# Performance work log

Measured on AMD Instinct MI355X. Metric: run time of the kernel, lower is better.

Reference implementation:

```python
import jax, jax.numpy as jnp
import numpy as np

B, N, C, H, D, K = 4, 8192, 384, 12, 2, 32
M = N // K            # 256 members per cluster
CH = C // H // 2      # 16 = q/k head dim (v gets 2*head_dim per the 6-way split)


def setup_inputs() -> dict:
    key = jax.random.key(0)
    ks = jax.random.split(key, 8)
    pos = jax.random.uniform(ks[0], (B, N, D), jnp.float32)
    feat = jax.random.normal(ks[1], (B, N, C), jnp.float32)
    # per-(b*h) row permutation of 0..N-1 -> clusters partition all tokens (cluster_mask=None path)
    perm_keys = jax.random.split(ks[2], B * H)
    member_idx = jax.vmap(lambda kk: jax.random.permutation(kk, N))(perm_keys).reshape(B * H, K, M)
    w_qkv = jax.random.normal(ks[3], (3 * C, C), jnp.float32) * (C ** -0.5)
    b_qkv = jnp.zeros((3 * C,), jnp.float32)
    w_pos = jax.random.normal(ks[4], (H, D), jnp.float32) * 0.1   # Conv1d(h*d->h, ksize 1, groups=h) weight squeezed
    b_pos = jnp.zeros((H,), jnp.float32)
    w_proj = jax.random.normal(ks[5], (C, 2 * C), jnp.float32) * ((2 * C) ** -0.5)
    b_proj = jnp.zeros((C,), jnp.float32)
    return {"pos": pos, "feat": feat, "member_idx": member_idx,
            "w_qkv": w_qkv, "b_qkv": b_qkv, "w_pos": w_pos, "b_pos": b_pos,
            "w_proj": w_proj, "b_proj": b_proj}


def reference(pos, feat, member_idx, w_qkv, b_qkv, w_pos, b_pos, w_proj, b_proj):
    b, n, c = feat.shape
    d = pos.shape[2]
    bh, k, m = member_idx.shape
    h = bh // b
    ch = c // h // 2
    scale = (c // h) ** -0.5

    # qkv projection -> (b*h, n, 6, ch)
    qkv = feat @ w_qkv.T + b_qkv                      # b n 3c
    qkv = qkv.reshape(b, n, h, 6, ch).transpose(0, 2, 1, 3, 4).reshape(bh, n, 6, ch)

    # gather cluster members -> (b*k, h, m, 6, ch)
    row = jnp.arange(bh)[:, None, None]
    g = qkv[row, member_idx]                          # bh k m 6 ch
    g = g.reshape(b, h, k, m, 6, ch).transpose(0, 2, 1, 3, 4, 5).reshape(b * k, h, m, 6, ch)
    q = g[:, :, :, 0] * scale                         # bk h m ch
    kk = g[:, :, :, 1]                                # bk h m ch
    v = g[:, :, :, 2:].reshape(b * k, h, m, 4 * ch)   # bk h m 2c_

    attn = jnp.einsum('khic,khjc->khij', q, kk)       # bk h m m (k axis = b*k)

    # positional bias: kernel-1 grouped conv is linear -> bias[i,j] = s_j - s_i + b_pos
    pos_n = pos / pos.reshape(-1, d).max(0)           # b n d
    pos_bh = jnp.repeat(pos_n, h, axis=0)             # bh n d
    pos_g = pos_bh[row, member_idx]                   # bh k m d
    pos_g = pos_g.reshape(b, h, k, m, d).transpose(0, 2, 1, 3, 4).reshape(b * k, h, m, d)
    s = jnp.einsum('khmd,hd->khm', pos_g, w_pos)      # bk h m
    pos_bias = s[:, :, None, :] - s[:, :, :, None] + b_pos[None, :, None, None]

    attn = jax.nn.softmax(attn + pos_bias, axis=-1)
    out = jnp.einsum('khij,khjc->khic', attn, v)      # bk h m 2c_

    # scatter back to original token order (member_idx is a permutation per row)
    out = out.reshape(b, k, h, m, 4 * ch).transpose(0, 2, 1, 3, 4).reshape(bh, k * m, 4 * ch)
    new_feat = jnp.zeros((bh, n, 4 * ch), out.dtype)
    new_feat = new_feat.at[jnp.arange(bh)[:, None], member_idx.reshape(bh, k * m)].set(out)
    feat2 = new_feat.reshape(b, h, n, 4 * ch).transpose(0, 2, 1, 3).reshape(b, n, 2 * c)

    return feat2 @ w_proj.T + b_proj                  # b n c
```

## Files before the change

kernel.cpp:

```cpp
#include <hip/hip_runtime.h>
#include <hip/hip_bf16.h>

#define B_  4
#define N_  8192
#define C_  384
#define H_  12
#define K_  32
#define M_  256
#define BN_ (B_*N_)
#define QKVD 1152
#define VSTR 260
#define LOG2E 1.4426950408889634f


typedef __attribute__((ext_vector_type(8)))  short  bf16x8;
typedef __attribute__((ext_vector_type(4)))  float  f32x4;
typedef __attribute__((ext_vector_type(16))) float  f32x16;
typedef __attribute__((ext_vector_type(4)))  ushort ushort4v;
typedef __attribute__((ext_vector_type(8)))  ushort ushort8v;

#define GLOBAL_AS __attribute__((address_space(1)))
#define LDS_AS    __attribute__((address_space(3)))

__device__ __forceinline__ void load_lds_16B(const ushort* g, ushort* l) {
    __builtin_amdgcn_global_load_lds((const GLOBAL_AS unsigned int*)g,
                                     (LDS_AS unsigned int*)l, 16, 0, 0);
}
__device__ __forceinline__ unsigned cvtpk_bf16(float lo, float hi) {
    unsigned r;
    asm("v_cvt_pk_bf16_f32 %0, %1, %2" : "=v"(r) : "v"(lo), "v"(hi));
    return r;
}
__device__ __forceinline__ float exp2_fast(float x) {
    float r;
    asm("v_exp_f32 %0, %1" : "=v"(r) : "v"(x));
    return r;
}
__device__ __forceinline__ float rcp_fast(float x) {
    float r;
    asm("v_rcp_f32 %0, %1" : "=v"(r) : "v"(x));
    return r;
}

__global__ void posmax_kernel(const float* __restrict__ pos, unsigned* __restrict__ pmax) {
    int tid = blockIdx.x * blockDim.x + threadIdx.x;
    float m0 = 0.f, m1 = 0.f;
    for (int i = tid; i < BN_; i += gridDim.x * blockDim.x) {
        m0 = fmaxf(m0, pos[(size_t)i * 2 + 0]);
        m1 = fmaxf(m1, pos[(size_t)i * 2 + 1]);
    }
    #pragma unroll
    for (int off = 32; off; off >>= 1) {
        m0 = fmaxf(m0, __shfl_down(m0, off));
        m1 = fmaxf(m1, __shfl_down(m1, off));
    }
    __shared__ float s0[4], s1[4];
    int w = threadIdx.x >> 6;
    if ((threadIdx.x & 63) == 0) { s0[w] = m0; s1[w] = m1; }
    __syncthreads();
    if (threadIdx.x == 0) {
        for (int i = 1; i < 4; i++) { m0 = fmaxf(m0, s0[i]); m1 = fmaxf(m1, s1[i]); }
        atomicMax(&pmax[0], __float_as_uint(m0));
        atomicMax(&pmax[1], __float_as_uint(m1));
    }
}

__global__ __launch_bounds__(256) void cast_kernel(const float* __restrict__ src,
                                                   ushort* __restrict__ dst, int n4) {
    int i = blockIdx.x * blockDim.x + threadIdx.x;
    if (i >= n4) return;
    float4 a = reinterpret_cast<const float4*>(src)[i];
    unsigned u01 = cvtpk_bf16(a.x, a.y), u23 = cvtpk_bf16(a.z, a.w);
    ushort4 o = { (ushort)(u01 & 0xffff), (ushort)(u01 >> 16),
                  (ushort)(u23 & 0xffff), (ushort)(u23 >> 16) };
    reinterpret_cast<ushort4*>(dst)[i] = o;
}

#define WQN 110592
#define WPN 73728
__global__ __launch_bounds__(256) void cast_w(const float* __restrict__ wq,
                                              const float* __restrict__ wp,
                                              ushort* __restrict__ wqb,
                                              ushort* __restrict__ wpb) {
    int i = blockIdx.x * 256 + threadIdx.x;
    const float* src; ushort* dst; int j;
    if (i < WQN) { src = wq; dst = wqb; j = i; }
    else         { src = wp; dst = wpb; j = i - WQN; }
    float4 a = reinterpret_cast<const float4*>(src)[j];
    unsigned u01 = cvtpk_bf16(a.x, a.y), u23 = cvtpk_bf16(a.z, a.w);
    ushort4 o = { (ushort)(u01 & 0xffff), (ushort)(u01 >> 16),
                  (ushort)(u23 & 0xffff), (ushort)(u23 >> 16) };
    reinterpret_cast<ushort4*>(dst)[j] = o;
}

__global__ __launch_bounds__(256) void gemm_qkv_s(const ushort* __restrict__ A,
                                                  const ushort* __restrict__ Bw,
                                                  const float* __restrict__ bias,
                                                  ushort* __restrict__ qkv) {
    constexpr int NB = QKVD / 128;
    __shared__ ushort As[128 * 64];
    __shared__ ushort Bs[128 * 64];
    const int wgid = blockIdx.x;
    const int xcd  = wgid & 7;
    const int loc  = wgid >> 3;
    const int bm = (xcd * 32 + loc / NB) * 128;
    const int bn = (loc % NB) * 128;
    const int t = threadIdx.x;
    const int l = t & 63;
    const int wr = (t >> 6) >> 1, wc = (t >> 6) & 1;
    const int fr = l & 15, fq = l >> 4;

    f32x4 zero = {0.f, 0.f, 0.f, 0.f};
    f32x4 acc[4][4];
    #pragma unroll
    for (int m = 0; m < 4; m++)
        #pragma unroll
        for (int n = 0; n < 4; n++) acc[m][n] = zero;

    for (int k0 = 0; k0 < 384; k0 += 64) {
        #pragma unroll
        for (int i = 0; i < 4; i++) {
            int elem = (i * 256 + t) * 8;
            int row = elem >> 6, kk = elem & 63;
            int kks = kk ^ ((row & 7) << 3);
            load_lds_16B(A + (size_t)(bm + row) * 384 + k0 + kks, &As[elem]);
        }
        #pragma unroll
        for (int i = 0; i < 4; i++) {
            int elem = (i * 256 + t) * 8;
            int row = elem >> 6, kk = elem & 63;
            int kks = kk ^ ((row & 7) << 3);
            load_lds_16B(Bw + (size_t)(bn + row) * 384 + k0 + kks, &Bs[elem]);
        }
        __syncthreads();
        #pragma unroll
        for (int kk = 0; kk < 64; kk += 32) {
            bf16x8 af[4], bfr[4];
            #pragma unroll
            for (int m = 0; m < 4; m++) {
                int row = wr * 64 + m * 16 + fr;
                af[m] = *reinterpret_cast<const bf16x8*>(&As[row * 64 + ((kk + fq * 8) ^ ((row & 7) << 3))]);
            }
            #pragma unroll
            for (int n = 0; n < 4; n++) {
                int row = wc * 64 + n * 16 + fr;
                bfr[n] = *reinterpret_cast<const bf16x8*>(&Bs[row * 64 + ((kk + fq * 8) ^ ((row & 7) << 3))]);
            }
            #pragma unroll
            for (int m = 0; m < 4; m++)
                #pragma unroll
                for (int n = 0; n < 4; n++)
                    acc[m][n] = __builtin_amdgcn_mfma_f32_16x16x32_bf16(af[m], bfr[n], acc[m][n], 0, 0, 0);
        }
        __syncthreads();
    }
    const int bq = bm >> 13;
    const int nbase = bm & (N_ - 1);
    #pragma unroll
    for (int n = 0; n < 4; n++) {
        int col = bn + wc * 64 + n * 16 + fr;
        int hc = col / 96, cn = col % 96;
        float bc = bias[col];
        ushort* base = qkv + ((size_t)(bq * H_ + hc) * N_ + nbase) * 96 + cn;
        #pragma unroll
        for (int m = 0; m < 4; m++) {
            #pragma unroll
            for (int r = 0; r < 4; r++) {
                int rowoff = wr * 64 + m * 16 + fq * 4 + r;
                __hip_bfloat16 hv = __float2bfloat16(acc[m][n][r] + bc);
                base[(size_t)rowoff * 96] = *(const ushort*)&hv;
            }
        }
    }
}

__global__ __launch_bounds__(512, 1) void attn_kernel(const ushort* __restrict__ qkv,
                                                      const int* __restrict__ member_idx,
                                                      const float* __restrict__ pos,
                                                      const float* __restrict__ w_pos,
                                                      const unsigned* __restrict__ pmax_u,
                                                      ushort* __restrict__ feat2) {
    const int id = blockIdx.x;
    const int bh = (id >> 8) * 8 + (id & 7);
    const int kc = (id >> 3) & 31;
    const int b = bh / H_, h = bh % H_;
    __shared__ ushort Ks[M_ * 16];
    __shared__ ushort Vt[64 * VSTR];
    __shared__ float  SpA[M_];
    __shared__ int    Idx[M_];
    __shared__ float  dinvS[8 * 32];

    const int t  = threadIdx.x;
    const int w  = t >> 6, l = t & 63;
    const int hi = l >> 5, ln = l & 31;
    const int* mi = member_idx + (((size_t)b * H_ + h) * K_ + kc) * M_;
    const ushort* slab = qkv + (size_t)bh * N_ * 96;
    const size_t rowbase = (size_t)b * N_;
    const float scale2 = 0.17677669529663687f * LOG2E;

    const int iq = 32 * w + ln;
    const int nq = mi[iq];
    bf16x8 qf = *(const bf16x8*)(slab + (size_t)nq * 96 + hi * 8);
    const int u = t >> 2, cq = t & 3;
    const int n0 = mi[2 * u], n1 = mi[2 * u + 1];
    const ushort* s0 = slab + (size_t)n0 * 96 + 32 + cq * 16;
    const ushort* s1 = slab + (size_t)n1 * 96 + 32 + cq * 16;
    ushort8v v0a = *(const ushort8v*)s0;
    ushort8v v0b = *(const ushort8v*)(s0 + 8);
    ushort8v v1a = *(const ushort8v*)s1;
    ushort8v v1b = *(const ushort8v*)(s1 + 8);
    {
        int row = t >> 1, half = t & 1;
        int n = mi[row];
        load_lds_16B(slab + (size_t)n * 96 + 16 + half * 8, &Ks[t * 8]);
    }
    if (t < M_) {
        int n = mi[t];
        Idx[t] = n;
        float inv0 = rcp_fast(__uint_as_float(pmax_u[0]));
        float inv1 = rcp_fast(__uint_as_float(pmax_u[1]));
        float sp = pos[(rowbase + n) * 2 + 0] * inv0 * w_pos[h * 2 + 0]
                 + pos[(rowbase + n) * 2 + 1] * inv1 * w_pos[h * 2 + 1];
        int jj = t & 31, jt = t >> 5;
        int r  = (jj & 3) | ((jj >> 3) << 2);
        int hb = (jj >> 2) & 1;
        SpA[jt * 32 + hb * 16 + r] = sp * LOG2E;
    }
    __syncthreads();

    f32x16 zero16;
    #pragma unroll
    for (int i = 0; i < 16; i++) zero16[i] = 0.f;
    f32x16 sac[8];
    __builtin_amdgcn_s_setprio(1);
    #pragma unroll
    for (int jt = 0; jt < 8; jt++) {
        bf16x8 kf = *(const bf16x8*)&Ks[(32 * jt + ln) * 16 + hi * 8];
        sac[jt] = __builtin_amdgcn_mfma_f32_32x32x16_bf16(kf, qf, zero16, 0, 0, 0);
    }
    __builtin_amdgcn_s_setprio(0);

    float mx = -3.0e38f;
    #pragma unroll
    for (int jt = 0; jt < 8; jt++) {
        f32x4 bia[4];
        #pragma unroll
        for (int q4 = 0; q4 < 4; q4++)
            bia[q4] = *(const f32x4*)&SpA[jt * 32 + hi * 16 + q4 * 4];
        #pragma unroll
        for (int r = 0; r < 16; r++)
            sac[jt][r] = fmaf(sac[jt][r], scale2, bia[r >> 2][r & 3]);
        #pragma unroll
        for (int r = 0; r < 16; r += 2)
            mx = fmaxf(mx, fmaxf(sac[jt][r], sac[jt][r + 1]));
    }
    mx = fmaxf(mx, __shfl_xor(mx, 32));
    float sum = 0.f;
    #pragma unroll
    for (int jt = 0; jt < 8; jt++)
        #pragma unroll
        for (int r = 0; r < 16; r++) {
            float p = exp2_fast(sac[jt][r] - mx);
            sac[jt][r] = p;
            sum += p;
        }
    sum += __shfl_xor(sum, 32);
    float inv = rcp_fast(sum);
    if (hi == 0) dinvS[w * 32 + ln] = inv;

    #pragma unroll
    for (int i = 0; i < 8; i++) {
        int c0 = cq * 16 + i, c1 = cq * 16 + 8 + i;
        *(unsigned*)&Vt[c0 * VSTR + 2 * u] = (unsigned)(ushort)v0a[i] | ((unsigned)(ushort)v1a[i] << 16);
        *(unsigned*)&Vt[c1 * VSTR + 2 * u] = (unsigned)(ushort)v0b[i] | ((unsigned)(ushort)v1b[i] << 16);
    }
    __syncthreads();

    f32x16 oa0 = zero16, oa1 = zero16;
    __builtin_amdgcn_s_setprio(1);
    #pragma unroll
    for (int g = 0; g < 16; g++) {
        const int jt = g >> 1, hf = (g & 1) * 8;
        unsigned a0 = cvtpk_bf16(sac[jt][hf + 0], sac[jt][hf + 1]);
        unsigned a1 = cvtpk_bf16(sac[jt][hf + 2], sac[jt][hf + 3]);
        unsigned b0 = cvtpk_bf16(sac[jt][hf + 4], sac[jt][hf + 5]);
        unsigned b1 = cvtpk_bf16(sac[jt][hf + 6], sac[jt][hf + 7]);
        asm("v_permlane32_swap_b32 %0, %1" : "+v"(a0), "+v"(b0));
        asm("v_permlane32_swap_b32 %0, %1" : "+v"(a1), "+v"(b1));
        union { unsigned uu[4]; bf16x8 v; } pa;
        pa.uu[0] = a0; pa.uu[1] = a1; pa.uu[2] = b0; pa.uu[3] = b1;
        union { ushort4v hv[2]; bf16x8 v; } vf0, vf1;
        vf0.hv[0] = *(const ushort4v*)&Vt[ln * VSTR + g * 16 + hi * 8];
        vf0.hv[1] = *(const ushort4v*)&Vt[ln * VSTR + g * 16 + hi * 8 + 4];
        vf1.hv[0] = *(const ushort4v*)&Vt[(ln + 32) * VSTR + g * 16 + hi * 8];
        vf1.hv[1] = *(const ushort4v*)&Vt[(ln + 32) * VSTR + g * 16 + hi * 8 + 4];
        oa0 = __builtin_amdgcn_mfma_f32_32x32x16_bf16(pa.v, vf0.v, oa0, 0, 0, 0);
        oa1 = __builtin_amdgcn_mfma_f32_32x32x16_bf16(pa.v, vf1.v, oa1, 0, 0, 0);
    }
    __builtin_amdgcn_s_setprio(0);

    ushort* f2slab = feat2 + (size_t)bh * N_ * 64;
    #pragma unroll
    for (int r = 0; r < 16; r++) {
        int crow = (r & 3) + 8 * (r >> 2) + 4 * hi;
        float dv = dinvS[w * 32 + crow];
        int ni = Idx[32 * w + crow];
        unsigned up = cvtpk_bf16(oa0[r] * dv, oa1[r] * dv);
        ushort* dst = f2slab + (size_t)ni * 64 + ln;
        dst[0]  = (ushort)(up & 0xffff);
        dst[32] = (ushort)(up >> 16);
    }
}

__global__ __launch_bounds__(256) void gemm_proj_s(const ushort* __restrict__ A,
                                                   const ushort* __restrict__ Bw,
                                                   const float* __restrict__ bias,
                                                   float* __restrict__ Cout) {
    constexpr int NB = C_ / 128;
    __shared__ ushort As[128 * 64];
    __shared__ ushort Bs[128 * 64];
    const int wgid = blockIdx.x;
    const int xcd  = wgid & 7;
    const int loc  = wgid >> 3;
    const int bm = (xcd * 32 + loc / NB) * 128;
    const int bn = (loc % NB) * 128;
    const int t = threadIdx.x;
    const int l = t & 63;
    const int wr = (t >> 6) >> 1, wc = (t >> 6) & 1;
    const int fr = l & 15, fq = l >> 4;
    const int bq = bm >> 13;
    const int nbase = bm & (N_ - 1);

    f32x4 zero = {0.f, 0.f, 0.f, 0.f};
    f32x4 acc[4][4];
    #pragma unroll
    for (int m = 0; m < 4; m++)
        #pragma unroll
        for (int n = 0; n < 4; n++) acc[m][n] = zero;

    for (int k0 = 0; k0 < 768; k0 += 64) {
        const ushort* Aslab = A + ((size_t)(bq * H_ + (k0 >> 6)) * N_ + nbase) * 64;
        #pragma unroll
        for (int i = 0; i < 4; i++) {
            int elem = (i * 256 + t) * 8;
            int row = elem >> 6, kk = elem & 63;
            int kks = kk ^ ((row & 7) << 3);
            load_lds_16B(Aslab + (size_t)row * 64 + kks, &As[elem]);
        }
        #pragma unroll
        for (int i = 0; i < 4; i++) {
            int elem = (i * 256 + t) * 8;
            int row = elem >> 6, kk = elem & 63;
            int kks = kk ^ ((row & 7) << 3);
            load_lds_16B(Bw + (size_t)(bn + row) * 768 + k0 + kks, &Bs[elem]);
        }
        __syncthreads();
        #pragma unroll
        for (int kk = 0; kk < 64; kk += 32) {
            bf16x8 af[4], bfr[4];
            #pragma unroll
            for (int m = 0; m < 4; m++) {
                int row = wr * 64 + m * 16 + fr;
                af[m] = *reinterpret_cast<const bf16x8*>(&As[row * 64 + ((kk + fq * 8) ^ ((row & 7) << 3))]);
            }
            #pragma unroll
            for (int n = 0; n < 4; n++) {
                int row = wc * 64 + n * 16 + fr;
                bfr[n] = *reinterpret_cast<const bf16x8*>(&Bs[row * 64 + ((kk + fq * 8) ^ ((row & 7) << 3))]);
            }
            #pragma unroll
            for (int m = 0; m < 4; m++)
                #pragma unroll
                for (int n = 0; n < 4; n++)
                    acc[m][n] = __builtin_amdgcn_mfma_f32_16x16x32_bf16(af[m], bfr[n], acc[m][n], 0, 0, 0);
        }
        __syncthreads();
    }
    #pragma unroll
    for (int n = 0; n < 4; n++) {
        int col = bn + wc * 64 + n * 16 + fr;
        float bc = bias[col];
        #pragma unroll
        for (int m = 0; m < 4; m++) {
            #pragma unroll
            for (int r = 0; r < 4; r++) {
                size_t row = bm + wr * 64 + m * 16 + fq * 4 + r;
                Cout[row * C_ + col] = acc[m][n][r] + bc;
            }
        }
    }
}

extern "C" void kernel_launch(void* const* d_in, const int* in_sizes, int n_in,
                              void* d_out, int out_size, void* d_ws, size_t ws_size,
                              hipStream_t stream) {
    const float* pos    = (const float*)d_in[0];
    const float* feat   = (const float*)d_in[1];
    const int*   midx   = (const int*)  d_in[2];
    const float* w_qkv  = (const float*)d_in[3];
    const float* b_qkv  = (const float*)d_in[4];
    const float* w_pos  = (const float*)d_in[5];
    const float* b_pos  = (const float*)d_in[6];  (void)b_pos;
    const float* w_proj = (const float*)d_in[7];
    const float* b_proj = (const float*)d_in[8];
    float* out = (float*)d_out;

    char* ws = (char*)d_ws;
    unsigned* pmax  = (unsigned*)ws;
    ushort*   qkv   = (ushort*)(ws + 256);
    ushort*   wproj = (ushort*)(ws + 256 + 75497472);
    char*     region = ws + 256 + 75497472 + 589824;
    ushort*   featb = (ushort*)region;
    ushort*   wqkvb = (ushort*)(region + 25165824);
    ushort*   feat2 = (ushort*)region;

    hipMemsetAsync(pmax, 0, 8, stream);
    posmax_kernel<<<64, 256, 0, stream>>>(pos, pmax);
    cast_kernel<<<(BN_ * C_ / 4 + 255) / 256, 256, 0, stream>>>(feat, featb, BN_ * C_ / 4);
    cast_w<<<(WQN + WPN) / 256, 256, 0, stream>>>(w_qkv, w_proj, wqkvb, wproj);
    gemm_qkv_s<<<8 * 32 * (QKVD / 128), 256, 0, stream>>>(featb, wqkvb, b_qkv, qkv);
    attn_kernel<<<6 * 256, 512, 0, stream>>>(qkv, midx, pos, w_pos, pmax, feat2);
    gemm_proj_s<<<8 * 32 * (C_ / 128), 256, 0, stream>>>(feat2, wproj, b_proj, out);
}
```

Baseline: 155.5 us.

## Halve attention block size, give each wave two query tiles, drop mid-kernel barrier

The attention kernel now runs 256 threads per block (4 waves) instead of 512, and each wave processes two 32-row query tiles in sequence. V is transposed into LDS before the first barrier, so the second __syncthreads between softmax and the PV matmul is gone. Launch bounds change to (256, 2) so two blocks can share a CU. The aim is to cut barrier stalls and per-block overhead and let independent blocks overlap. In exchange each wave does more serial work and holds more registers, since both Q fragments stay live.

```diff
diff --git a/kernel.cpp b/kernel.cpp
--- a/kernel.cpp
+++ b/kernel.cpp
@@ -174,7 +174,7 @@
     }
 }
 
-__global__ __launch_bounds__(512, 1) void attn_kernel(const ushort* __restrict__ qkv,
+__global__ __launch_bounds__(256, 2) void attn_kernel(const ushort* __restrict__ qkv,
                                                       const int* __restrict__ member_idx,
                                                       const float* __restrict__ pos,
                                                       const float* __restrict__ w_pos,
@@ -188,7 +188,7 @@
     __shared__ ushort Vt[64 * VSTR];
     __shared__ float  SpA[M_];
     __shared__ int    Idx[M_];
-    __shared__ float  dinvS[8 * 32];
+    __shared__ float  dinvS[M_];
 
     const int t  = threadIdx.x;
     const int w  = t >> 6, l = t & 63;
@@ -198,23 +198,38 @@
     const size_t rowbase = (size_t)b * N_;
     const float scale2 = 0.17677669529663687f * LOG2E;
 
-    const int iq = 32 * w + ln;
-    const int nq = mi[iq];
-    bf16x8 qf = *(const bf16x8*)(slab + (size_t)nq * 96 + hi * 8);
-    const int u = t >> 2, cq = t & 3;
-    const int n0 = mi[2 * u], n1 = mi[2 * u + 1];
-    const ushort* s0 = slab + (size_t)n0 * 96 + 32 + cq * 16;
-    const ushort* s1 = slab + (size_t)n1 * 96 + 32 + cq * 16;
-    ushort8v v0a = *(const ushort8v*)s0;
-    ushort8v v0b = *(const ushort8v*)(s0 + 8);
-    ushort8v v1a = *(const ushort8v*)s1;
-    ushort8v v1b = *(const ushort8v*)(s1 + 8);
+    const int nq0 = mi[w * 64 + ln];
+    const int nq1 = mi[w * 64 + 32 + ln];
+    bf16x8 qf0 = *(const bf16x8*)(slab + (size_t)nq0 * 96 + hi * 8);
+    bf16x8 qf1 = *(const bf16x8*)(slab + (size_t)nq1 * 96 + hi * 8);
+    #pragma unroll
+    for (int it = 0; it < 2; it++) {
+        int idx = it * 256 + t;
+        int row = idx >> 1, half = idx & 1;
+        int n = mi[row];
+        load_lds_16B(slab + (size_t)n * 96 + 16 + half * 8, &Ks[idx * 8]);
+    }
     {
-        int row = t >> 1, half = t & 1;
-        int n = mi[row];
-        load_lds_16B(slab + (size_t)n * 96 + 16 + half * 8, &Ks[t * 8]);
-    }
-    if (t < M_) {
+        int u = t >> 1, cqh = t & 1;
+        int n0 = mi[2 * u], n1 = mi[2 * u + 1];
+        #pragma unroll
+        for (int qq = 0; qq < 2; qq++) {
+            int cq = 2 * cqh + qq;
+            const ushort* s0 = slab + (size_t)n0 * 96 + 32 + cq * 16;
+            const ushort* s1 = slab + (size_t)n1 * 96 + 32 + cq * 16;
+            ushort8v v0a = *(const ushort8v*)s0;
+            ushort8v v0b = *(const ushort8v*)(s0 + 8);
+            ushort8v v1a = *(const ushort8v*)s1;
+            ushort8v v1b = *(const ushort8v*)(s1 + 8);
+            #pragma unroll
+            for (int i = 0; i < 8; i++) {
+                int c0 = cq * 16 + i, c1 = cq * 16 + 8 + i;
+                *(unsigned*)&Vt[c0 * VSTR + 2 * u] = (unsigned)(ushort)v0a[i] | ((unsigned)(ushort)v1a[i] << 16);
+                *(unsigned*)&Vt[c1 * VSTR + 2 * u] = (unsigned)(ushort)v0b[i] | ((unsigned)(ushort)v1b[i] << 16);
+            }
+        }
+    }
+    {
         int n = mi[t];
         Idx[t] = n;
         float inv0 = rcp_fast(__uint_as_float(pmax_u[0]));
@@ -231,84 +246,83 @@
     f32x16 zero16;
     #pragma unroll
     for (int i = 0; i < 16; i++) zero16[i] = 0.f;
-    f32x16 sac[8];
-    __builtin_amdgcn_s_setprio(1);
-    #pragma unroll
-    for (int jt = 0; jt < 8; jt++) {
-        bf16x8 kf = *(const bf16x8*)&Ks[(32 * jt + ln) * 16 + hi * 8];
-        sac[jt] = __builtin_amdgcn_mfma_f32_32x32x16_bf16(kf, qf, zero16, 0, 0, 0);
-    }
-    __builtin_amdgcn_s_setprio(0);
-
-    float mx = -3.0e38f;
-    #pragma unroll
-    for (int jt = 0; jt < 8; jt++) {
-        f32x4 bia[4];
-        #pragma unroll
-        for (int q4 = 0; q4 < 4; q4++)
-            bia[q4] = *(const f32x4*)&SpA[jt * 32 + hi * 16 + q4 * 4];
-        #pragma unroll
-        for (int r = 0; r < 16; r++)
-            sac[jt][r] = fmaf(sac[jt][r], scale2, bia[r >> 2][r & 3]);
-        #pragma unroll
-        for (int r = 0; r < 16; r += 2)
-            mx = fmaxf(mx, fmaxf(sac[jt][r], sac[jt][r + 1]));
-    }
-    mx = fmaxf(mx, __shfl_xor(mx, 32));
-    float sum = 0.f;
-    #pragma unroll
-    for (int jt = 0; jt < 8; jt++)
+    ushort* f2slab = feat2 + (size_t)bh * N_ * 64;
+
+    #pragma unroll
+    for (int p = 0; p < 2; p++) {
+        const int qb = w * 64 + p * 32;
+        const bf16x8 qf = p ? qf1 : qf0;
+
+        f32x16 sac[8];
+        __builtin_amdgcn_s_setprio(1);
+        #pragma unroll
+        for (int jt = 0; jt < 8; jt++) {
+            bf16x8 kf = *(const bf16x8*)&Ks[(32 * jt + ln) * 16 + hi * 8];
+            sac[jt] = __builtin_amdgcn_mfma_f32_32x32x16_bf16(kf, qf, zero16, 0, 0, 0);
+        }
+        __builtin_amdgcn_s_setprio(0);
+
+        float mx = -3.0e38f;
+        #pragma unroll
+        for (int jt = 0; jt < 8; jt++) {
+            f32x4 bia[4];
+            #pragma unroll
+            for (int q4 = 0; q4 < 4; q4++)
+                bia[q4] = *(const f32x4*)&SpA[jt * 32 + hi * 16 + q4 * 4];
+            #pragma unroll
+            for (int r = 0; r < 16; r++)
+                sac[jt][r] = fmaf(sac[jt][r], scale2, bia[r >> 2][r & 3]);
+            #pragma unroll
+            for (int r = 0; r < 16; r += 2)
+                mx = fmaxf(mx, fmaxf(sac[jt][r], sac[jt][r + 1]));
+        }
+        mx = fmaxf(mx, __shfl_xor(mx, 32));
+        float sum = 0.f;
+        #pragma unroll
+        for (int jt = 0; jt < 8; jt++)
+            #pragma unroll
+            for (int r = 0; r < 16; r++) {
+                float pv = exp2_fast(sac[jt][r] - mx);
+                sac[jt][r] = pv;
+                sum += pv;
+            }
+        sum += __shfl_xor(sum, 32);
+        float inv = rcp_fast(sum);
+        if (hi == 0) dinvS[qb + ln] = inv;
+
+        f32x16 oa0 = zero16, oa1 = zero16;
+        __builtin_amdgcn_s_setprio(1);
+        #pragma unroll
+        for (int g = 0; g < 16; g++) {
+            const int jt = g >> 1, hf = (g & 1) * 8;
+            unsigned a0 = cvtpk_bf16(sac[jt][hf + 0], sac[jt][hf + 1]);
+            unsigned a1 = cvtpk_bf16(sac[jt][hf + 2], sac[jt][hf + 3]);
+            unsigned b0 = cvtpk_bf16(sac[jt][hf + 4], sac[jt][hf + 5]);
+            unsigned b1 = cvtpk_bf16(sac[jt][hf + 6], sac[jt][hf + 7]);
+            asm("v_permlane32_swap_b32 %0, %1" : "+v"(a0), "+v"(b0));
+            asm("v_permlane32_swap_b32 %0, %1" : "+v"(a1), "+v"(b1));
+            union { unsigned uu[4]; bf16x8 v; } pa;
+            pa.uu[0] = a0; pa.uu[1] = a1; pa.uu[2] = b0; pa.uu[3] = b1;
+            union { ushort4v hv[2]; bf16x8 v; } vf0, vf1;
+            vf0.hv[0] = *(const ushort4v*)&Vt[ln * VSTR + g * 16 + hi * 8];
+            vf0.hv[1] = *(const ushort4v*)&Vt[ln * VSTR + g * 16 + hi * 8 + 4];
+            vf1.hv[0] = *(const ushort4v*)&Vt[(ln + 32) * VSTR + g * 16 + hi * 8];
+            vf1.hv[1] = *(const ushort4v*)&Vt[(ln + 32) * VSTR + g * 16 + hi * 8 + 4];
+            oa0 = __builtin_amdgcn_mfma_f32_32x32x16_bf16(pa.v, vf0.v, oa0, 0, 0, 0);
+            oa1 = __builtin_amdgcn_mfma_f32_32x32x16_bf16(pa.v, vf1.v, oa1, 0, 0, 0);
+        }
+        __builtin_amdgcn_s_setprio(0);
+
         #pragma unroll
         for (int r = 0; r < 16; r++) {
-            float p = exp2_fast(sac[jt][r] - mx);
-            sac[jt][r] = p;
-            sum += p;
-        }
-    sum += __shfl_xor(sum, 32);
-    float inv = rcp_fast(sum);
-    if (hi == 0) dinvS[w * 32 + ln] = inv;
-
-    #pragma unroll
-    for (int i = 0; i < 8; i++) {
-        int c0 = cq * 16 + i, c1 = cq * 16 + 8 + i;
-        *(unsigned*)&Vt[c0 * VSTR + 2 * u] = (unsigned)(ushort)v0a[i] | ((unsigned)(ushort)v1a[i] << 16);
-        *(unsigned*)&Vt[c1 * VSTR + 2 * u] = (unsigned)(ushort)v0b[i] | ((unsigned)(ushort)v1b[i] << 16);
-    }
-    __syncthreads();
-
-    f32x16 oa0 = zero16, oa1 = zero16;
-    __builtin_amdgcn_s_setprio(1);
-    #pragma unroll
-    for (int g = 0; g < 16; g++) {
-        const int jt = g >> 1, hf = (g & 1) * 8;
-        unsigned a0 = cvtpk_bf16(sac[jt][hf + 0], sac[jt][hf + 1]);
-        unsigned a1 = cvtpk_bf16(sac[jt][hf + 2], sac[jt][hf + 3]);
-        unsigned b0 = cvtpk_bf16(sac[jt][hf + 4], sac[jt][hf + 5]);
-        unsigned b1 = cvtpk_bf16(sac[jt][hf + 6], sac[jt][hf + 7]);
-        asm("v_permlane32_swap_b32 %0, %1" : "+v"(a0), "+v"(b0));
-        asm("v_permlane32_swap_b32 %0, %1" : "+v"(a1), "+v"(b1));
-        union { unsigned uu[4]; bf16x8 v; } pa;
-        pa.uu[0] = a0; pa.uu[1] = a1; pa.uu[2] = b0; pa.uu[3] = b1;
-        union { ushort4v hv[2]; bf16x8 v; } vf0, vf1;
-        vf0.hv[0] = *(const ushort4v*)&Vt[ln * VSTR + g * 16 + hi * 8];
-        vf0.hv[1] = *(const ushort4v*)&Vt[ln * VSTR + g * 16 + hi * 8 + 4];
-        vf1.hv[0] = *(const ushort4v*)&Vt[(ln + 32) * VSTR + g * 16 + hi * 8];
-        vf1.hv[1] = *(const ushort4v*)&Vt[(ln + 32) * VSTR + g * 16 + hi * 8 + 4];
-        oa0 = __builtin_amdgcn_mfma_f32_32x32x16_bf16(pa.v, vf0.v, oa0, 0, 0, 0);
-        oa1 = __builtin_amdgcn_mfma_f32_32x32x16_bf16(pa.v, vf1.v, oa1, 0, 0, 0);
-    }
-    __builtin_amdgcn_s_setprio(0);
-
-    ushort* f2slab = feat2 + (size_t)bh * N_ * 64;
-    #pragma unroll
-    for (int r = 0; r < 16; r++) {
-        int crow = (r & 3) + 8 * (r >> 2) + 4 * hi;
-        float dv = dinvS[w * 32 + crow];
-        int ni = Idx[32 * w + crow];
-        unsigned up = cvtpk_bf16(oa0[r] * dv, oa1[r] * dv);
-        ushort* dst = f2slab + (size_t)ni * 64 + ln;
-        dst[0]  = (ushort)(up & 0xffff);
-        dst[32] = (ushort)(up >> 16);
+            int crow = (r & 3) + 8 * (r >> 2) + 4 * hi;
+            float dv = dinvS[qb + crow];
+            int ni = Idx[qb + crow];
+            unsigned up = cvtpk_bf16(oa0[r] * dv, oa1[r] * dv);
+            ushort* dst = f2slab + (size_t)ni * 64 + ln;
+            dst[0]  = (ushort)(up & 0xffff);
+            dst[32] = (ushort)(up >> 16);
+        }
     }
 }
 
@@ -419,6 +433,6 @@
     cast_kernel<<<(BN_ * C_ / 4 + 255) / 256, 256, 0, stream>>>(feat, featb, BN_ * C_ / 4);
     cast_w<<<(WQN + WPN) / 256, 256, 0, stream>>>(w_qkv, w_proj, wqkvb, wproj);
     gemm_qkv_s<<<8 * 32 * (QKVD / 128), 256, 0, stream>>>(featb, wqkvb, b_qkv, qkv);
-    attn_kernel<<<6 * 256, 512, 0, stream>>>(qkv, midx, pos, w_pos, pmax, feat2);
+    attn_kernel<<<6 * 256, 256, 0, stream>>>(qkv, midx, pos, w_pos, pmax, feat2);
     gemm_proj_s<<<8 * 32 * (C_ / 128), 256, 0, stream>>>(feat2, wproj, b_proj, out);
 }
```

Result: faster. 148.4 us (-4.6%).
